# Kernel optimization log

Measured on AMD Instinct MI355X. Metric: run time of the kernel, lower is better.

## Reference

```python
import jax, jax.numpy as jnp
import numpy as np

D_MODEL = 1024
N_HEADS = 16
MLP_DIM = 4096


def _layernorm(x, g, b, eps=1e-5):
    mu = jnp.mean(x, axis=-1, keepdims=True)
    var = jnp.var(x, axis=-1, keepdims=True)
    return (x - mu) * jax.lax.rsqrt(var + eps) * g + b


def setup_inputs() -> dict:
    key = jax.random.key(0)
    ks = jax.random.split(key, 12)
    B, S, D, F = 2, 2048, D_MODEL, MLP_DIM
    s = 1.0 / np.sqrt(D)
    sf = 1.0 / np.sqrt(F)
    return {
        "x": jax.random.normal(ks[0], (B, S, D), jnp.float32),
        "ln1_g": jnp.ones((D,), jnp.float32),
        "ln1_b": jnp.zeros((D,), jnp.float32),
        "w_q": jax.random.uniform(ks[1], (D, D), jnp.float32, -s, s),
        "w_k": jax.random.uniform(ks[2], (D, D), jnp.float32, -s, s),
        "w_v": jax.random.uniform(ks[3], (D, D), jnp.float32, -s, s),
        "w_o": jax.random.uniform(ks[4], (D, D), jnp.float32, -s, s),
        "b_o": jax.random.uniform(ks[5], (D,), jnp.float32, -s, s),
        "ln2_g": jnp.ones((D,), jnp.float32),
        "ln2_b": jnp.zeros((D,), jnp.float32),
        "w1": jax.random.uniform(ks[6], (D, F), jnp.float32, -s, s),
        "b1": jax.random.uniform(ks[7], (F,), jnp.float32, -s, s),
        "w2": jax.random.uniform(ks[8], (F, D), jnp.float32, -sf, sf),
        "b2": jax.random.uniform(ks[9], (D,), jnp.float32, -sf, sf),
    }


def reference(x, ln1_g, ln1_b, w_q, w_k, w_v, w_o, b_o, ln2_g, ln2_b, w1, b1, w2, b2):
    B, S, D = x.shape
    H = N_HEADS
    hd = D // H
    # --- attention sublayer (pre-LN, residual) ---
    h = _layernorm(x, ln1_g, ln1_b)
    q = (h @ w_q).reshape(B, S, H, hd).transpose(0, 2, 1, 3)  # [B,H,S,hd]
    k = (h @ w_k).reshape(B, S, H, hd).transpose(0, 2, 1, 3)
    v = (h @ w_v).reshape(B, S, H, hd).transpose(0, 2, 1, 3)
    scores = jnp.einsum('bhqd,bhkd->bhqk', q, k) / np.sqrt(hd)  # [B,H,S,S]
    attn = jax.nn.softmax(scores, axis=-1)
    out = jnp.einsum('bhqk,bhkd->bhqd', attn, v)
    out = out.transpose(0, 2, 1, 3).reshape(B, S, D)
    x = out @ w_o + b_o + x
    # --- MLP sublayer (pre-LN, residual) ---
    h = _layernorm(x, ln2_g, ln2_b)
    h = jax.nn.gelu(h @ w1 + b1, approximate=False)
    return h @ w2 + b2 + x
```

## Files before the change

### kernel.cpp

```cpp
#include <hip/hip_runtime.h>
#include <math.h>


typedef __attribute__((ext_vector_type(8))) short s8v;
typedef __attribute__((ext_vector_type(4))) short s4v;
typedef __attribute__((ext_vector_type(4))) float f4v;
typedef __attribute__((ext_vector_type(16))) float f16v;

#define M_ROWS 4096
#define DM 1024
#define FF 4096
#define QKV_LD 3072

__device__ inline short f2bf(float f) {
  unsigned u = __builtin_bit_cast(unsigned, f);
  u += 0x7fff + ((u >> 16) & 1);
  return (short)(u >> 16);
}

__device__ inline void gload_lds16(const void* g, void* lds) {
  __builtin_amdgcn_global_load_lds(
      (const __attribute__((address_space(1))) unsigned*)(uintptr_t)g,
      (__attribute__((address_space(3))) unsigned*)(unsigned)(uintptr_t)lds,
      16, 0, 0);
}

__device__ inline s4v ds_tr16(unsigned off) {
  s4v r;
  asm volatile("ds_read_b64_tr_b16 %0, %1" : "=v"(r) : "v"(off));
  return r;
}

__device__ inline s8v cat8(s4v a, s4v b) {
  return __builtin_shufflevector(a, b, 0, 1, 2, 3, 4, 5, 6, 7);
}

__device__ inline unsigned pkbf(float a, float b) {
  unsigned r;
  asm("v_cvt_pk_bf16_f32 %0, %1, %2" : "=v"(r) : "v"(a), "v"(b));
  return r;
}

__device__ inline float gelu_t(float x) {
  float x3 = x * x * x;
  float z = fmaf(x3, 0.044715f, x) * 1.5957691216f;
  float e = __expf(z);
  float th = fmaf(-2.0f, __frcp_rn(e + 1.0f), 1.0f);
  return 0.5f * x * (1.0f + th);
}

__global__ void wt_kernel(const float* __restrict__ W, short* __restrict__ Wt,
                          int K, int N) {
  __shared__ float tile[32][33];
  int tx = threadIdx.x, ty = threadIdx.y;
  int n0 = blockIdx.x * 32, k0 = blockIdx.y * 32;
#pragma unroll
  for (int i = 0; i < 4; ++i)
    tile[ty + 8 * i][tx] = W[(size_t)(k0 + ty + 8 * i) * N + n0 + tx];
  __syncthreads();
#pragma unroll
  for (int i = 0; i < 4; ++i)
    Wt[(size_t)(n0 + ty + 8 * i) * K + k0 + tx] = f2bf(tile[tx][ty + 8 * i]);
}

__global__ __launch_bounds__(256) void ln_kernel(const float* __restrict__ x,
                                                 const float* __restrict__ g,
                                                 const float* __restrict__ b,
                                                 short* __restrict__ out) {
  int row = blockIdx.x, tid = threadIdx.x;
  const float4* xr = (const float4*)(x + (size_t)row * DM);
  float4 v = xr[tid];
  float s = v.x + v.y + v.z + v.w;
  float q = v.x * v.x + v.y * v.y + v.z * v.z + v.w * v.w;
#pragma unroll
  for (int off = 32; off; off >>= 1) {
    s += __shfl_down(s, off);
    q += __shfl_down(q, off);
  }
  __shared__ float red[8];
  if ((tid & 63) == 0) { red[tid >> 6] = s; red[4 + (tid >> 6)] = q; }
  __syncthreads();
  if (tid == 0) {
    float S = red[0] + red[1] + red[2] + red[3];
    float Q = red[4] + red[5] + red[6] + red[7];
    float mean = S * (1.0f / DM);
    float var = Q * (1.0f / DM) - mean * mean;
    red[0] = mean;
    red[1] = rsqrtf(var + 1e-5f);
  }
  __syncthreads();
  float mean = red[0], rstd = red[1];
  float4 gv = ((const float4*)g)[tid], bv = ((const float4*)b)[tid];
  s4v o;
  o[0] = f2bf((v.x - mean) * rstd * gv.x + bv.x);
  o[1] = f2bf((v.y - mean) * rstd * gv.y + bv.y);
  o[2] = f2bf((v.z - mean) * rstd * gv.z + bv.z);
  o[3] = f2bf((v.w - mean) * rstd * gv.w + bv.w);
  *(s4v*)&out[(size_t)row * DM + tid * 4] = o;
}

template <int EPI>
__global__ __launch_bounds__(256) void gemm_kernel(
    const short* __restrict__ A, const short* __restrict__ Bt,
    const float* __restrict__ bias, const float* __restrict__ res,
    void* __restrict__ Cout, int M, int N, int K) {
  __shared__ short As[2][128 * 64];
  __shared__ short Bs[2][128 * 64];
  int tid = threadIdx.x, lane = tid & 63, wave = tid >> 6;
  int wr = wave >> 1, wc = wave & 1;
  int l16 = lane & 15, lhi = lane >> 4;
  int row0 = blockIdx.y * 128, col0 = blockIdx.x * 128;
  int lrow = lane >> 3, lcol8 = (lane & 7) * 8;

  const f4v fzero = {0.f, 0.f, 0.f, 0.f};
  f4v acc[4][4];
#pragma unroll
  for (int m = 0; m < 4; ++m)
#pragma unroll
    for (int n = 0; n < 4; ++n) acc[m][n] = fzero;

  const int nt = K >> 6;

#pragma unroll
  for (int i = 0; i < 4; ++i) {
    int ch = wave * 4 + i;
    int row = ch * 8 + lrow;
    gload_lds16(&A[(size_t)(row0 + row) * K + lcol8], &As[0][ch * 512]);
    gload_lds16(&Bt[(size_t)(col0 + row) * K + lcol8], &Bs[0][ch * 512]);
  }
  __syncthreads();

  for (int t = 0; t < nt; ++t) {
    int cur = t & 1, nxt = cur ^ 1;
    if (t + 1 < nt) {
      int k1 = (t + 1) << 6;
#pragma unroll
      for (int i = 0; i < 4; ++i) {
        int ch = wave * 4 + i;
        int row = ch * 8 + lrow;
        gload_lds16(&A[(size_t)(row0 + row) * K + k1 + lcol8], &As[nxt][ch * 512]);
        gload_lds16(&Bt[(size_t)(col0 + row) * K + k1 + lcol8], &Bs[nxt][ch * 512]);
      }
    }
#pragma unroll
    for (int kk = 0; kk < 2; ++kk) {
      s8v af[4], bfr[4];
#pragma unroll
      for (int m = 0; m < 4; ++m)
        af[m] = *(const s8v*)&As[cur][(wr * 64 + m * 16 + l16) * 64 + kk * 32 + lhi * 8];
#pragma unroll
      for (int n = 0; n < 4; ++n)
        bfr[n] = *(const s8v*)&Bs[cur][(wc * 64 + n * 16 + l16) * 64 + kk * 32 + lhi * 8];
#pragma unroll
      for (int m = 0; m < 4; ++m)
#pragma unroll
        for (int n = 0; n < 4; ++n)
          acc[m][n] = __builtin_amdgcn_mfma_f32_16x16x32_bf16(af[m], bfr[n],
                                                              acc[m][n], 0, 0, 0);
    }
    __syncthreads();
  }

#pragma unroll
  for (int m = 0; m < 4; ++m)
#pragma unroll
    for (int n = 0; n < 4; ++n)
#pragma unroll
      for (int r = 0; r < 4; ++r) {
        int row = row0 + wr * 64 + m * 16 + lhi * 4 + r;
        int col = col0 + wc * 64 + n * 16 + l16;
        size_t idx = (size_t)row * N + col;
        float v = acc[m][n][r];
        if (EPI == 0) {
          ((short*)Cout)[idx] = f2bf(v);
        } else if (EPI == 1) {
          ((float*)Cout)[idx] = v + bias[col] + res[idx];
        } else {
          ((short*)Cout)[idx] = f2bf(gelu_t(v + bias[col]));
        }
      }
}

__global__ __launch_bounds__(256) void attn_kernel(const short* __restrict__ q,
                                                   const short* __restrict__ k,
                                                   const short* __restrict__ v,
                                                   short* __restrict__ o) {
  __shared__ short Ks[64 * 64];
  __shared__ short Vt[64 * 64];
  int tid = threadIdx.x, lane = tid & 63, w = tid >> 6;
  int l31 = lane & 31, l15 = lane & 15, h = lane >> 5;
  int qb = blockIdx.x * 128;
  int bh = blockIdx.y;
  int b = bh >> 4, hh = bh & 15;
  const size_t rbase = (size_t)b * 2048 * QKV_LD + (size_t)hh * 64;
  unsigned vtb = (unsigned)(uintptr_t)&Vt[0];

  int qrow = qb + w * 32 + l31;
  s8v qf[4];
#pragma unroll
  for (int c = 0; c < 4; ++c)
    qf[c] = *(const s8v*)&q[rbase + (size_t)qrow * QKV_LD + c * 16 + h * 8];

  f16v o0, o1;
#pragma unroll
  for (int i = 0; i < 16; ++i) { o0[i] = 0.f; o1[i] = 0.f; }
  float mreg = -3.0e38f, lsum = 0.f;

  for (int kt = 0; kt < 2048; kt += 64) {
    __syncthreads();
#pragma unroll
    for (int i = 0; i < 2; ++i) {
      int ch = w * 2 + i;
      {
        int row = ch * 8 + (lane >> 3);
        int cs = lane & 7;
        int col = ((cs ^ (row & 7)) * 8);
        gload_lds16(&k[rbase + (size_t)(kt + row) * QKV_LD + col], &Ks[ch * 512]);
      }
      {
        int nb = ch >> 1, rem = (ch & 1) * 64 + lane;
        int key = rem >> 1, c8 = rem & 1;
        gload_lds16(&v[rbase + (size_t)(kt + key) * QKV_LD + nb * 16 + c8 * 8],
                    &Vt[ch * 512]);
      }
    }
    __syncthreads();

    f16v t0, t1;
#pragma unroll
    for (int i = 0; i < 16; ++i) { t0[i] = 0.f; t1[i] = 0.f; }
    __builtin_amdgcn_s_setprio(1);
#pragma unroll
    for (int c = 0; c < 4; ++c) {
      int slot = ((2 * c + h) ^ (l31 & 7)) * 8;
      s8v k0f = *(const s8v*)&Ks[l31 * 64 + slot];
      s8v k1f = *(const s8v*)&Ks[(32 + l31) * 64 + slot];
      t0 = __builtin_amdgcn_mfma_f32_32x32x16_bf16(k0f, qf[c], t0, 0, 0, 0);
      t1 = __builtin_amdgcn_mfma_f32_32x32x16_bf16(k1f, qf[c], t1, 0, 0, 0);
    }
    __builtin_amdgcn_s_setprio(0);

    float mx[8];
#pragma unroll
    for (int i = 0; i < 8; ++i)
      mx[i] = fmaxf(fmaxf(t0[i], t0[i + 8]), fmaxf(t1[i], t1[i + 8]));
    float rm = fmaxf(fmaxf(fmaxf(mx[0], mx[1]), fmaxf(mx[2], mx[3])),
                     fmaxf(fmaxf(mx[4], mx[5]), fmaxf(mx[6], mx[7])));
    rm = fmaxf(rm, __shfl_xor(rm, 32));
    float newm = fmaxf(mreg, rm);
    float sc = __expf((mreg - newm) * 0.125f);
    float ms = newm * 0.125f;
    mreg = newm;
#pragma unroll
    for (int i = 0; i < 16; ++i) {
      t0[i] = __expf(fmaf(t0[i], 0.125f, -ms));
      t1[i] = __expf(fmaf(t1[i], 0.125f, -ms));
    }
    float sm[8];
#pragma unroll
    for (int i = 0; i < 8; ++i)
      sm[i] = (t0[i] + t0[i + 8]) + (t1[i] + t1[i + 8]);
    float rs = ((sm[0] + sm[1]) + (sm[2] + sm[3])) +
               ((sm[4] + sm[5]) + (sm[6] + sm[7]));
    rs += __shfl_xor(rs, 32);
    lsum = lsum * sc + rs;

    s8v pB[4];
#pragma unroll
    for (int c = 0; c < 4; ++c) {
      int rb = (c & 1) * 8;
      float e0, e1, e2, e3, e4, e5, e6, e7;
      if (c < 2) {
        e0 = t0[rb]; e1 = t0[rb + 1]; e2 = t0[rb + 2]; e3 = t0[rb + 3];
        e4 = t0[rb + 4]; e5 = t0[rb + 5]; e6 = t0[rb + 6]; e7 = t0[rb + 7];
      } else {
        e0 = t1[rb]; e1 = t1[rb + 1]; e2 = t1[rb + 2]; e3 = t1[rb + 3];
        e4 = t1[rb + 4]; e5 = t1[rb + 5]; e6 = t1[rb + 6]; e7 = t1[rb + 7];
      }
      unsigned wA0 = pkbf(e0, e1), wA1 = pkbf(e2, e3);
      unsigned wB0 = pkbf(e4, e5), wB1 = pkbf(e6, e7);
      unsigned s0 = h ? wA0 : wB0, s1 = h ? wA1 : wB1;
      unsigned r0 = __shfl_xor(s0, 32), r1 = __shfl_xor(s1, 32);
      uint4 ww;
      ww.x = h ? r0 : wA0;
      ww.y = h ? r1 : wA1;
      ww.z = h ? wB0 : r0;
      ww.w = h ? wB1 : r1;
      pB[c] = __builtin_bit_cast(s8v, ww);
    }

    s4v va[2][4][2];
#pragma unroll
    for (int db = 0; db < 2; ++db) {
      unsigned base = vtb + (unsigned)(db * 2 + (l31 >> 4)) * 2048 + 2u * l15;
#pragma unroll
      for (int c = 0; c < 4; ++c) {
        unsigned a = base + (unsigned)(c * 512 + h * 256);
        va[db][c][0] = ds_tr16(a);
        va[db][c][1] = ds_tr16(a + 128);
      }
    }
#pragma unroll
    for (int i = 0; i < 16; ++i) { o0[i] *= sc; o1[i] *= sc; }
    asm volatile("s_waitcnt lgkmcnt(0)");
    __builtin_amdgcn_sched_barrier(0);
    __builtin_amdgcn_s_setprio(1);
#pragma unroll
    for (int c = 0; c < 4; ++c) {
      o0 = __builtin_amdgcn_mfma_f32_32x32x16_bf16(cat8(va[0][c][0], va[0][c][1]),
                                                   pB[c], o0, 0, 0, 0);
      o1 = __builtin_amdgcn_mfma_f32_32x32x16_bf16(cat8(va[1][c][0], va[1][c][1]),
                                                   pB[c], o1, 0, 0, 0);
    }
    __builtin_amdgcn_s_setprio(0);
  }

  float inv = 1.0f / lsum;
  size_t obase = ((size_t)b * 2048 + qrow) * 1024 + hh * 64;
#pragma unroll
  for (int db = 0; db < 2; ++db)
#pragma unroll
    for (int qq = 0; qq < 4; ++qq) {
      s4v pv;
#pragma unroll
      for (int i = 0; i < 4; ++i) {
        float val = (db == 0 ? o0[qq * 4 + i] : o1[qq * 4 + i]) * inv;
        pv[i] = f2bf(val);
      }
      *(s4v*)&o[obase + db * 32 + qq * 8 + h * 4] = pv;
    }
}

extern "C" void kernel_launch(void* const* d_in, const int* in_sizes, int n_in,
                              void* d_out, int out_size, void* d_ws, size_t ws_size,
                              hipStream_t stream) {
  (void)in_sizes; (void)n_in; (void)out_size; (void)ws_size;
  const float* x    = (const float*)d_in[0];
  const float* ln1g = (const float*)d_in[1];
  const float* ln1b = (const float*)d_in[2];
  const float* wq   = (const float*)d_in[3];
  const float* wk   = (const float*)d_in[4];
  const float* wv   = (const float*)d_in[5];
  const float* wo   = (const float*)d_in[6];
  const float* bo   = (const float*)d_in[7];
  const float* ln2g = (const float*)d_in[8];
  const float* ln2b = (const float*)d_in[9];
  const float* w1   = (const float*)d_in[10];
  const float* b1   = (const float*)d_in[11];
  const float* w2   = (const float*)d_in[12];
  const float* b2   = (const float*)d_in[13];
  float* out = (float*)d_out;

  char* ws = (char*)d_ws;
  const size_t MB = 1024 * 1024;
  short* h1   = (short*)(ws);
  short* qkv  = (short*)(ws + 8 * MB);
  short* mid  = (short*)(ws);
  short* at   = (short*)(ws + 32 * MB);
  short* h2   = (short*)(ws + 32 * MB);
  float* x2   = (float*)(ws + 40 * MB);
  short* wqkvT = (short*)(ws + 56 * MB);
  short* wqT  = wqkvT;
  short* wkT  = wqkvT + 1024 * 1024;
  short* wvT  = wqkvT + 2 * 1024 * 1024;
  short* woT  = (short*)(ws + 62 * MB);
  short* w1T  = (short*)(ws + 64 * MB);
  short* w2T  = (short*)(ws + 72 * MB);

  dim3 tb(32, 8);
  wt_kernel<<<dim3(32, 32), tb, 0, stream>>>(wq, wqT, 1024, 1024);
  wt_kernel<<<dim3(32, 32), tb, 0, stream>>>(wk, wkT, 1024, 1024);
  wt_kernel<<<dim3(32, 32), tb, 0, stream>>>(wv, wvT, 1024, 1024);
  wt_kernel<<<dim3(32, 32), tb, 0, stream>>>(wo, woT, 1024, 1024);
  wt_kernel<<<dim3(128, 32), tb, 0, stream>>>(w1, w1T, 1024, 4096);
  wt_kernel<<<dim3(32, 128), tb, 0, stream>>>(w2, w2T, 4096, 1024);

  ln_kernel<<<M_ROWS, 256, 0, stream>>>(x, ln1g, ln1b, h1);

  gemm_kernel<0><<<dim3(24, 32), 256, 0, stream>>>(h1, wqkvT, nullptr, nullptr,
                                                   qkv, M_ROWS, QKV_LD, DM);

  attn_kernel<<<dim3(16, 32), 256, 0, stream>>>(qkv, qkv + 1024, qkv + 2048, at);

  gemm_kernel<1><<<dim3(8, 32), 256, 0, stream>>>(at, woT, bo, x, x2, M_ROWS, DM, DM);

  ln_kernel<<<M_ROWS, 256, 0, stream>>>(x2, ln2g, ln2b, h2);

  gemm_kernel<2><<<dim3(32, 32), 256, 0, stream>>>(h2, w1T, b1, nullptr, mid,
                                                   M_ROWS, FF, DM);

  gemm_kernel<1><<<dim3(8, 32), 256, 0, stream>>>(mid, w2T, b2, x2, out,
                                                  M_ROWS, DM, FF);
}
```

Before: 277.4 us.

## Double-buffer K/V tiles in attention and skip online-softmax rescales lazily

The attention kernel now keeps two LDS buffers for K and V. It issues the global-to-LDS loads for the next 64-key tile before computing the current one, so load latency overlaps the MFMA and softmax work, and each iteration needs one barrier instead of two. The output and row-sum rescale only runs when some lane's tile max exceeds the running max by more than a threshold, so most iterations skip the 32 multiplies and an exp. The softmax exponentials use exp2f with the 1/sqrt(d)·log2(e) scale folded into a single FMA. The cost is double the LDS footprint and possibly larger unnormalised exponentials, which stay bounded by the threshold.

```diff
diff --git a/kernel.cpp b/kernel.cpp
--- a/kernel.cpp
+++ b/kernel.cpp
@@ -185,15 +185,36 @@
                                                    const short* __restrict__ k,
                                                    const short* __restrict__ v,
                                                    short* __restrict__ o) {
-  __shared__ short Ks[64 * 64];
-  __shared__ short Vt[64 * 64];
+  __shared__ short Ks[2][64 * 64];
+  __shared__ short Vt[2][64 * 64];
   int tid = threadIdx.x, lane = tid & 63, w = tid >> 6;
   int l31 = lane & 31, l15 = lane & 15, h = lane >> 5;
   int qb = blockIdx.x * 128;
   int bh = blockIdx.y;
   int b = bh >> 4, hh = bh & 15;
   const size_t rbase = (size_t)b * 2048 * QKV_LD + (size_t)hh * 64;
-  unsigned vtb = (unsigned)(uintptr_t)&Vt[0];
+  const float S2 = 0.18033688f;
+
+  int ch0 = w * 2, ch1 = w * 2 + 1;
+  int krow0 = ch0 * 8 + (lane >> 3), krow1 = ch1 * 8 + (lane >> 3);
+  int kcol0 = (((lane & 7) ^ (krow0 & 7)) * 8);
+  int kcol1 = (((lane & 7) ^ (krow1 & 7)) * 8);
+  int vnb0 = ch0 >> 1, vnb1 = ch1 >> 1;
+  int vrem0 = (ch0 & 1) * 64 + lane, vrem1 = (ch1 & 1) * 64 + lane;
+  int vkey0 = vrem0 >> 1, vc80 = vrem0 & 1;
+  int vkey1 = vrem1 >> 1, vc81 = vrem1 & 1;
+
+#define STAGE_KV(buf, kt)                                                      \
+  {                                                                            \
+    gload_lds16(&k[rbase + (size_t)((kt) + krow0) * QKV_LD + kcol0],           \
+                &Ks[buf][ch0 * 512]);                                          \
+    gload_lds16(&k[rbase + (size_t)((kt) + krow1) * QKV_LD + kcol1],           \
+                &Ks[buf][ch1 * 512]);                                          \
+    gload_lds16(&v[rbase + (size_t)((kt) + vkey0) * QKV_LD + vnb0 * 16 + vc80 * 8], \
+                &Vt[buf][ch0 * 512]);                                          \
+    gload_lds16(&v[rbase + (size_t)((kt) + vkey1) * QKV_LD + vnb1 * 16 + vc81 * 8], \
+                &Vt[buf][ch1 * 512]);                                          \
+  }
 
   int qrow = qb + w * 32 + l31;
   s8v qf[4];
@@ -206,25 +227,13 @@
   for (int i = 0; i < 16; ++i) { o0[i] = 0.f; o1[i] = 0.f; }
   float mreg = -3.0e38f, lsum = 0.f;
 
-  for (int kt = 0; kt < 2048; kt += 64) {
-    __syncthreads();
-#pragma unroll
-    for (int i = 0; i < 2; ++i) {
-      int ch = w * 2 + i;
-      {
-        int row = ch * 8 + (lane >> 3);
-        int cs = lane & 7;
-        int col = ((cs ^ (row & 7)) * 8);
-        gload_lds16(&k[rbase + (size_t)(kt + row) * QKV_LD + col], &Ks[ch * 512]);
-      }
-      {
-        int nb = ch >> 1, rem = (ch & 1) * 64 + lane;
-        int key = rem >> 1, c8 = rem & 1;
-        gload_lds16(&v[rbase + (size_t)(kt + key) * QKV_LD + nb * 16 + c8 * 8],
-                    &Vt[ch * 512]);
-      }
-    }
-    __syncthreads();
+  STAGE_KV(0, 0);
+  __syncthreads();
+
+  for (int t = 0; t < 32; ++t) {
+    int cur = t & 1;
+    if (t + 1 < 32) STAGE_KV(cur ^ 1, (t + 1) * 64);
+    unsigned vtb = (unsigned)(uintptr_t)&Vt[cur][0];
 
     f16v t0, t1;
 #pragma unroll
@@ -233,8 +242,8 @@
 #pragma unroll
     for (int c = 0; c < 4; ++c) {
       int slot = ((2 * c + h) ^ (l31 & 7)) * 8;
-      s8v k0f = *(const s8v*)&Ks[l31 * 64 + slot];
-      s8v k1f = *(const s8v*)&Ks[(32 + l31) * 64 + slot];
+      s8v k0f = *(const s8v*)&Ks[cur][l31 * 64 + slot];
+      s8v k1f = *(const s8v*)&Ks[cur][(32 + l31) * 64 + slot];
       t0 = __builtin_amdgcn_mfma_f32_32x32x16_bf16(k0f, qf[c], t0, 0, 0, 0);
       t1 = __builtin_amdgcn_mfma_f32_32x32x16_bf16(k1f, qf[c], t1, 0, 0, 0);
     }
@@ -247,14 +256,19 @@
     float rm = fmaxf(fmaxf(fmaxf(mx[0], mx[1]), fmaxf(mx[2], mx[3])),
                      fmaxf(fmaxf(mx[4], mx[5]), fmaxf(mx[6], mx[7])));
     rm = fmaxf(rm, __shfl_xor(rm, 32));
-    float newm = fmaxf(mreg, rm);
-    float sc = __expf((mreg - newm) * 0.125f);
-    float ms = newm * 0.125f;
-    mreg = newm;
+    if (!__all(rm <= mreg + 64.0f)) {
+      float newm = fmaxf(mreg, rm);
+      float sc = exp2f((mreg - newm) * S2);
+      mreg = newm;
+#pragma unroll
+      for (int i = 0; i < 16; ++i) { o0[i] *= sc; o1[i] *= sc; }
+      lsum *= sc;
+    }
+    float ms2 = mreg * S2;
 #pragma unroll
     for (int i = 0; i < 16; ++i) {
-      t0[i] = __expf(fmaf(t0[i], 0.125f, -ms));
-      t1[i] = __expf(fmaf(t1[i], 0.125f, -ms));
+      t0[i] = exp2f(fmaf(t0[i], S2, -ms2));
+      t1[i] = exp2f(fmaf(t1[i], S2, -ms2));
     }
     float sm[8];
 #pragma unroll
@@ -263,7 +277,7 @@
     float rs = ((sm[0] + sm[1]) + (sm[2] + sm[3])) +
                ((sm[4] + sm[5]) + (sm[6] + sm[7]));
     rs += __shfl_xor(rs, 32);
-    lsum = lsum * sc + rs;
+    lsum += rs;
 
     s8v pB[4];
 #pragma unroll
@@ -300,8 +314,6 @@
         va[db][c][1] = ds_tr16(a + 128);
       }
     }
-#pragma unroll
-    for (int i = 0; i < 16; ++i) { o0[i] *= sc; o1[i] *= sc; }
     asm volatile("s_waitcnt lgkmcnt(0)");
     __builtin_amdgcn_sched_barrier(0);
     __builtin_amdgcn_s_setprio(1);
@@ -313,6 +325,7 @@
                                                    pB[c], o1, 0, 0, 0);
     }
     __builtin_amdgcn_s_setprio(0);
+    __syncthreads();
   }
 
   float inv = 1.0f / lsum;
@@ -329,6 +342,7 @@
       }
       *(s4v*)&o[obase + db * 32 + qq * 8 + h * 4] = pv;
     }
+#undef STAGE_KV
 }
 
 extern "C" void kernel_launch(void* const* d_in, const int* in_sizes, int n_in,
```

New measurement: 279.4 us. No clear change (+0.7%).
